# Kernel optimization log

Hardware: AMD Instinct MI355X
Metric: run time of the kernel (lower is better)

## Reference

```python
import jax, jax.numpy as jnp
from jax import lax
import numpy as np

EPS = 1e-6
D_KQ = 256  # per-head q/k dim; softmax scale = sqrt(256) = 16


def layernorm(x, g, b):
    m = jnp.mean(x, axis=-1, keepdims=True)
    v = jnp.var(x, axis=-1, keepdims=True)  # biased, matches torch LayerNorm
    return (x - m) / jnp.sqrt(v + EPS) * g + b


def lrelu(t):
    return jnp.where(t > 0, t, 0.1 * t)


def setup_inputs() -> dict:
    key = jax.random.key(0)
    ks = jax.random.split(key, 10)
    B, C, H, W = 256, 17, 84, 84
    d_model, heads = 512, 4
    hid = D_KQ * heads  # 1024
    out_dim = 256
    s = 0.05
    return {
        "x": jax.random.normal(ks[0], (B, C, H, W), jnp.float32),
        "conv1_w": jax.random.normal(ks[1], (64, C, 8, 8), jnp.float32) * s,
        "conv1_b": jnp.zeros((64,), jnp.float32),
        "conv2_w": jax.random.normal(ks[2], (510, 64, 4, 4), jnp.float32) * s,
        "conv2_b": jnp.zeros((510,), jnp.float32),
        "wq": jax.random.normal(ks[3], (hid, d_model), jnp.float32) * s,
        "wk": jax.random.normal(ks[4], (hid, d_model), jnp.float32) * s,
        "wv": jax.random.normal(ks[5], (hid, d_model), jnp.float32) * s,
        "ln_e_g": jnp.ones((hid,), jnp.float32),
        "ln_e_b": jnp.zeros((hid,), jnp.float32),
        "wo": jax.random.normal(ks[6], (d_model, hid), jnp.float32) * s,
        "ln_g": jnp.ones((d_model,), jnp.float32),
        "ln_b": jnp.zeros((d_model,), jnp.float32),
        "map_w": jax.random.normal(ks[7], (out_dim, d_model), jnp.float32) * s,
        "map_b": jnp.zeros((out_dim,), jnp.float32),
    }


def reference(x, conv1_w, conv1_b, conv2_w, conv2_b, wq, wk, wv,
              ln_e_g, ln_e_b, wo, ln_g, ln_b, map_w, map_b):
    dn = ("NCHW", "OIHW", "NCHW")
    # feature extractor
    y = lax.conv_general_dilated(x, conv1_w, (4, 4), "VALID", dimension_numbers=dn)
    y = lrelu(y + conv1_b[None, :, None, None])
    y = lax.conv_general_dilated(y, conv2_w, (2, 2), "VALID", dimension_numbers=dn)
    y = lrelu(y + conv2_b[None, :, None, None])  # [B,510,H2,W2]
    B, Cc, H2, W2 = y.shape
    N = H2 * W2
    e = jnp.transpose(y.reshape(B, Cc, N), (0, 2, 1))  # [B,N,510]
    # coordinate augmentation: [(i//W)/H, (i%W)/W]
    idx = jnp.arange(N)
    coord = jnp.stack([(idx // W2) / H2, (idx % W2) / W2], axis=-1).astype(e.dtype)
    e = jnp.concatenate([e, jnp.broadcast_to(coord, (B, N, 2))], axis=-1)  # [B,N,512]
    heads = 4
    # projections + per-projection LayerNorm over full hid dim (pre-head-split)
    q = layernorm(e @ wq.T, ln_e_g, ln_e_b).reshape(B, N, heads, D_KQ)
    k = layernorm(e @ wk.T, ln_e_g, ln_e_b).reshape(B, N, heads, D_KQ)
    v = layernorm(e @ wv.T, ln_e_g, ln_e_b).reshape(B, N, heads, D_KQ)
    scores = jnp.einsum("bnhd,bmhd->bhnm", q, k) / jnp.sqrt(jnp.float32(D_KQ))
    w = jax.nn.softmax(scores, axis=-1)
    nv = jnp.einsum("bhnm,bmhd->bnhd", w, v).reshape(B, N, heads * D_KQ)
    out = layernorm(nv @ wo.T + e, ln_g, ln_b)  # residual + LN
    out = jax.nn.relu(out)
    out = jnp.max(out, axis=1)  # maxout over entities -> [B,512]
    return lrelu(out @ map_w.T + map_b)  # mapping -> [B,256]
```

## Files before the change

### kernel.cpp

```cpp
#include <hip/hip_runtime.h>
#include <hip/hip_bf16.h>
#include <math.h>

typedef __hip_bfloat16 bf16;
using f32x4 = __attribute__((ext_vector_type(4))) float;
using s16x8 = __attribute__((ext_vector_type(8))) short;

#define DEV_INLINE __device__ __forceinline__

static constexpr int BB   = 256;
static constexpr int CIN  = 17;
static constexpr int WIN  = 84;
static constexpr int C1   = 64;
static constexpr int W1   = 20;
static constexpr int P1   = W1 * W1;
static constexpr int C2   = 510;
static constexpr int W2   = 9;
static constexpr int NE   = 81;
static constexpr int DM   = 512;
static constexpr int HID  = 1024;
static constexpr int NH   = 4;
static constexpr int DK   = 256;
static constexpr int MR   = BB * NE;
static constexpr int ODIM = 256;
static constexpr int PLANE = WIN * WIN;
static constexpr int QS   = 3 * HID;

DEV_INLINE float lrelu_f(float v) { return v > 0.f ? v : 0.1f * v; }
DEV_INLINE float bf2f(ushort u) { return __uint_as_float((unsigned)u << 16); }
DEV_INLINE short f2bs(float f) { bf16 t = __float2bfloat16(f); return *reinterpret_cast<short*>(&t); }

DEV_INLINE void gll16(const void* g, const void* l) {
    __builtin_amdgcn_global_load_lds(
        (const __attribute__((address_space(1))) unsigned int*)g,
        (__attribute__((address_space(3))) unsigned int*)l, 16, 0, 0);
}
DEV_INLINE f32x4 mfma16(s16x8 a, s16x8 b, f32x4 c) {
    return __builtin_amdgcn_mfma_f32_16x16x32_bf16(a, b, c, 0, 0, 0);
}

__global__ void k_prep(const float* __restrict__ w1, const float* __restrict__ w2,
        const float* __restrict__ b2, const float* __restrict__ wq,
        const float* __restrict__ wk, const float* __restrict__ wv,
        const float* __restrict__ wo, bf16* __restrict__ w1b,
        bf16* __restrict__ w2b, float* __restrict__ b2p,
        bf16* __restrict__ wqkv, bf16* __restrict__ wob) {
    int i = blockIdx.x * 256 + threadIdx.x;
    if (i < 17408) {
        const size_t o = (size_t)i * 4;
        const float4 v = *(const float4*)(w1 + o);
        short r[4] = { f2bs(v.x), f2bs(v.y), f2bs(v.z), f2bs(v.w) };
        *(ushort4*)(w1b + o) = *(ushort4*)r;
        return;
    }
    i -= 17408;
    if (i < 524288) {
        const int n = i >> 10, rem = i & 1023;
        const int khkw = rem >> 6, ic = rem & 63;
        w2b[i] = (n < C2) ? __float2bfloat16(w2[n * 1024 + ic * 16 + khkw])
                          : __float2bfloat16(0.f);
        return;
    }
    i -= 524288;
    if (i < 512) { b2p[i] = (i < C2) ? b2[i] : 0.f; return; }
    i -= 512;
    if (i < 393216) {
        const size_t o = (size_t)i * 4;
        const int n = (int)(o >> 9), c = (int)(o & 511);
        const float* src = (n < 1024) ? wq : (n < 2048) ? wk : wv;
        const float4 v = *(const float4*)(src + (size_t)(n & 1023) * 512 + c);
        short r[4] = { f2bs(v.x), f2bs(v.y), f2bs(v.z), f2bs(v.w) };
        *(ushort4*)(wqkv + o) = *(ushort4*)r;
        return;
    }
    i -= 393216;
    if (i < 131072) {
        const size_t o = (size_t)i * 4;
        const float4 v = *(const float4*)(wo + o);
        short r[4] = { f2bs(v.x), f2bs(v.y), f2bs(v.z), f2bs(v.w) };
        *(ushort4*)(wob + o) = *(ushort4*)r;
    }
}

__global__ __launch_bounds__(512, 1) void k_conv1_mfma(const float* __restrict__ x,
        const bf16* __restrict__ w1b, const float* __restrict__ bias,
        bf16* __restrict__ y1t) {
    __shared__ __align__(16) char pl[2][28224];
    const int b = blockIdx.x;
    const int tid = threadIdx.x;
    const int w = tid >> 6, l = tid & 63;
    const int l15 = l & 15, l4 = l >> 4;
    const float* xb = x + (size_t)b * CIN * PLANE;

    int baseA[4], tval[4];
    #pragma unroll
    for (int j = 0; j < 4; ++j) {
        const int t = w + 8 * j; tval[j] = t;
        int p = t * 16 + l15; if (t >= 25) p = 0;
        const int oh = p / 20, ow = p % 20;
        baseA[j] = (oh * 4 + l4) * 336 + ow * 16;
    }
    float bias_r[4];
    #pragma unroll
    for (int nt = 0; nt < 4; ++nt) bias_r[nt] = bias[nt * 16 + l15];

    #pragma unroll
    for (int it = 0; it < 4; ++it) {
        const int g = it * 512 + tid;
        if (g < 1764) gll16(xb + (size_t)g * 4, pl[0] + (size_t)g * 16);
    }
    __syncthreads();

    f32x4 acc[4][4] = {};
    int cur = 0;
    for (int ic = 0; ic < CIN; ++ic) {
        if (ic + 1 < CIN) {
            const float* src = xb + (size_t)(ic + 1) * PLANE;
            #pragma unroll
            for (int it = 0; it < 4; ++it) {
                const int g = it * 512 + tid;
                if (g < 1764) gll16(src + (size_t)g * 4, pl[cur ^ 1] + (size_t)g * 16);
            }
        }
        s16x8 bq[4][2];
        #pragma unroll
        for (int nt = 0; nt < 4; ++nt)
            #pragma unroll
            for (int ks = 0; ks < 2; ++ks)
                bq[nt][ks] = *(const s16x8*)(w1b + (size_t)(nt * 16 + l15) * 1088
                                             + ic * 64 + (ks * 4 + l4) * 8);
        const char* P = pl[cur];
        #pragma unroll
        for (int j = 0; j < 4; ++j) {
            if (tval[j] < 25) {
                #pragma unroll
                for (int ks = 0; ks < 2; ++ks) {
                    const float* fp = (const float*)(P + baseA[j] + ks * 1344);
                    const f32x4 f0 = *(const f32x4*)fp;
                    const f32x4 f1 = *(const f32x4*)(fp + 4);
                    s16x8 af;
                    #pragma unroll
                    for (int jj = 0; jj < 4; ++jj) {
                        af[jj]     = f2bs(f0[jj]);
                        af[jj + 4] = f2bs(f1[jj]);
                    }
                    #pragma unroll
                    for (int nt = 0; nt < 4; ++nt)
                        acc[j][nt] = mfma16(af, bq[nt][ks], acc[j][nt]);
                }
            }
        }
        __syncthreads();
        cur ^= 1;
    }
    #pragma unroll
    for (int j = 0; j < 4; ++j) {
        if (tval[j] < 25) {
            #pragma unroll
            for (int nt = 0; nt < 4; ++nt) {
                #pragma unroll
                for (int q = 0; q < 4; ++q) {
                    const int pix = tval[j] * 16 + l4 * 4 + q;
                    const int oc  = nt * 16 + l15;
                    y1t[((size_t)b * P1 + pix) * 64 + oc] =
                        __float2bfloat16(lrelu_f(acc[j][nt][q] + bias_r[nt]));
                }
            }
        }
    }
}

__global__ __launch_bounds__(256) void k_gemm_conv2(const bf16* __restrict__ A,
        const bf16* __restrict__ B, const float* __restrict__ bias,
        bf16* __restrict__ Cb) {
    __shared__ __align__(16) char Asm[2][128 * 64];
    __shared__ __align__(16) char Bsm[2][128 * 64];
    const int tid = threadIdx.x;
    const int m0 = blockIdx.y * 128, n0 = blockIdx.x * 128;
    const int w = tid >> 6, l = tid & 63;
    const int wm = w >> 1, wn = w & 1;
    const int l15 = l & 15, l4 = l >> 4;
    const int r0 = tid >> 2, p0 = tid & 3;
    const int r1 = 64 + r0;
    const int sw0 = (p0 ^ ((r0 >> 1) & 3)) << 3;
    const int sw1 = (p0 ^ ((r1 >> 1) & 3)) << 3;
    int bimg[2], ohh[2], oww[2];
    #pragma unroll
    for (int it = 0; it < 2; ++it) {
        const int m = m0 + (it ? r1 : r0);
        bimg[it] = m / 81;
        const int n = m - bimg[it] * 81;
        ohh[it] = n / 9; oww[it] = n - ohh[it] * 9;
    }
    auto stage = [&](int buf, int k0) {
        const int khkw = k0 >> 6, icb = k0 & 63;
        const int kh = khkw >> 2, kwv = khkw & 3;
        const int pix0 = (ohh[0] * 2 + kh) * 20 + oww[0] * 2 + kwv;
        const int pix1 = (ohh[1] * 2 + kh) * 20 + oww[1] * 2 + kwv;
        gll16(A + ((size_t)bimg[0] * P1 + pix0) * 64 + icb + sw0, Asm[buf] + tid * 16);
        gll16(A + ((size_t)bimg[1] * P1 + pix1) * 64 + icb + sw1, Asm[buf] + (256 + tid) * 16);
        gll16(B + (size_t)(n0 + r0) * HID + k0 + sw0, Bsm[buf] + tid * 16);
        gll16(B + (size_t)(n0 + r1) * HID + k0 + sw1, Bsm[buf] + (256 + tid) * 16);
    };
    stage(0, 0);
    __syncthreads();
    f32x4 acc[4][4] = {};
    int cur = 0;
    for (int t = 0; t < 32; ++t) {
        if (t < 31) stage(cur ^ 1, (t + 1) * 32);
        s16x8 af[4], bfv[4];
        #pragma unroll
        for (int i = 0; i < 4; ++i) {
            const int ra = wm * 64 + i * 16 + l15;
            af[i]  = *(const s16x8*)(Asm[cur] + ra * 64 + ((l4 ^ ((ra >> 1) & 3)) << 4));
            const int rb = wn * 64 + i * 16 + l15;
            bfv[i] = *(const s16x8*)(Bsm[cur] + rb * 64 + ((l4 ^ ((rb >> 1) & 3)) << 4));
        }
        #pragma unroll
        for (int i = 0; i < 4; ++i)
            #pragma unroll
            for (int j = 0; j < 4; ++j)
                acc[i][j] = mfma16(af[i], bfv[j], acc[i][j]);
        __syncthreads();
        cur ^= 1;
    }
    #pragma unroll
    for (int i = 0; i < 4; ++i) {
        #pragma unroll
        for (int j = 0; j < 4; ++j) {
            const int col = n0 + wn * 64 + j * 16 + l15;
            #pragma unroll
            for (int q = 0; q < 4; ++q) {
                const int row = m0 + wm * 64 + i * 16 + l4 * 4 + q;
                float v = lrelu_f(acc[i][j][q] + bias[col]);
                if (col >= 510) {
                    const int n = row % 81;
                    v = (col == 510) ? (float)(n / 9) * (1.f / 9.f)
                                     : (float)(n % 9) * (1.f / 9.f);
                }
                Cb[(size_t)row * DM + col] = __float2bfloat16(v);
            }
        }
    }
}

#define QKV_PHASE(QD, STAGING, TAIL)                                           \
    {                                                                          \
        s16x8 areg[2][2];                                                      \
        _Pragma("unroll")                                                      \
        for (int ii = 0; ii < 2; ++ii) {                                       \
            const int fr = QD * 32 + ii * 16 + l15;                            \
            _Pragma("unroll")                                                  \
            for (int kk = 0; kk < 2; ++kk)                                     \
                areg[ii][kk] = *(const s16x8*)(Abase + fr * 128 +              \
                                   (((kk * 4 + l4) ^ (fr & 7)) << 4));         \
        }                                                                      \
        STAGING;                                                               \
        __builtin_amdgcn_s_barrier();                                          \
        asm volatile("s_waitcnt lgkmcnt(0)" ::: "memory");                     \
        __builtin_amdgcn_sched_barrier(0);                                     \
        __builtin_amdgcn_s_setprio(1);                                         \
        _Pragma("unroll")                                                      \
        for (int ii = 0; ii < 2; ++ii)                                         \
            _Pragma("unroll")                                                  \
            for (int j = 0; j < 4; ++j)                                        \
                _Pragma("unroll")                                              \
                for (int kk = 0; kk < 2; ++kk)                                 \
                    acc[QD * 2 + ii][j] =                                      \
                        mfma16(areg[ii][kk], breg[j][kk], acc[QD * 2 + ii][j]);\
        __builtin_amdgcn_s_setprio(0);                                         \
        TAIL;                                                                  \
        __builtin_amdgcn_s_barrier();                                          \
        __builtin_amdgcn_sched_barrier(0);                                     \
    }

__global__ __launch_bounds__(512, 2) void k_gemm_qkv8(const bf16* __restrict__ A,
        const bf16* __restrict__ B, bf16* __restrict__ Cb,
        float2* __restrict__ part) {
    __shared__ __align__(16) char lds[131072];
    const int tid = threadIdx.x;
    const int m0 = blockIdx.y * 256, n0 = blockIdx.x * 256;
    const int wid = tid >> 6, l = tid & 63;
    const int wm = wid >> 2, wn = wid & 3;
    const int l15 = l & 15, l4 = l >> 4;
    const int rA = tid >> 3, pA = tid & 7;

    auto stageA = [&](int buf, int kt, int qa) {
        char* dst = lds + buf * 32768 + (qa >> 1) * 16384 + (qa & 1) * 8192 + tid * 16;
        gll16(A + (size_t)(m0 + qa * 64 + rA) * 512 + kt * 64 + ((pA ^ (rA & 7)) << 3), dst);
    };
    auto stageB = [&](int buf, int kt, int hb) {
        char* base = lds + 65536 + buf * 32768 + hb * 16384;
        #pragma unroll
        for (int i2 = 0; i2 < 2; ++i2) {
            const int s = i2 * 512 + tid;
            const int c = s >> 3, pp = s & 7;
            gll16(B + (size_t)(n0 + hb * 128 + c) * 512 + kt * 64 + ((pp ^ (c & 7)) << 3),
                  base + s * 16);
        }
    };

    stageA(0, 0, 0); stageA(0, 0, 1); stageA(0, 0, 2); stageA(0, 0, 3);
    stageB(0, 0, 0); stageB(0, 0, 1);
    stageB(1, 1, 0); stageB(1, 1, 1);
    stageA(1, 1, 0); stageA(1, 1, 2);
    asm volatile("s_waitcnt vmcnt(6)" ::: "memory");
    __builtin_amdgcn_s_barrier();
    __builtin_amdgcn_sched_barrier(0);

    f32x4 acc[8][4] = {};
    for (int kt = 0; kt < 8; ++kt) {
        const int cur = kt & 1;
        const char* Abase = lds + cur * 32768 + wm * 16384;
        const char* Bbase = lds + 65536 + cur * 32768 + (wn >> 1) * 16384;
        s16x8 breg[4][2];
        #pragma unroll
        for (int j = 0; j < 4; ++j) {
            const int fc = (wn & 1) * 64 + j * 16 + l15;
            #pragma unroll
            for (int kk = 0; kk < 2; ++kk)
                breg[j][kk] = *(const s16x8*)(Bbase + fc * 128 +
                                  (((kk * 4 + l4) ^ (fc & 7)) << 4));
        }
        QKV_PHASE(0, { if (kt + 1 < 8) { stageA(cur ^ 1, kt + 1, 1); stageA(cur ^ 1, kt + 1, 3); } }, {})
        QKV_PHASE(1, { if (kt + 2 < 8) { stageB(cur, kt + 2, 0); } }, {})
        QKV_PHASE(2, { if (kt + 2 < 8) { stageB(cur, kt + 2, 1); stageA(cur, kt + 2, 0); stageA(cur, kt + 2, 2); } }, {})
        QKV_PHASE(3, { }, {
            if (kt < 6)       { asm volatile("s_waitcnt vmcnt(6)" ::: "memory"); }
            else if (kt == 6) { asm volatile("s_waitcnt vmcnt(0)" ::: "memory"); }
        })
    }

    #pragma unroll
    for (int fi = 0; fi < 8; ++fi) {
        #pragma unroll
        for (int q = 0; q < 4; ++q) {
            const int row = m0 + wm * 128 + fi * 16 + l4 * 4 + q;
            float s = 0.f, s2 = 0.f;
            #pragma unroll
            for (int j = 0; j < 4; ++j) {
                const float v = acc[fi][j][q];
                s += v; s2 += v * v;
            }
            #pragma unroll
            for (int o = 1; o < 16; o <<= 1) {
                s  += __shfl_xor(s, o, 64);
                s2 += __shfl_xor(s2, o, 64);
            }
            if (l15 == 0)
                part[(size_t)row * 48 + blockIdx.x * 4 + wn] = make_float2(s, s2);
            bf16* cr = Cb + (size_t)row * QS + n0 + wn * 64;
            #pragma unroll
            for (int j = 0; j < 4; ++j)
                cr[j * 16 + l15] = __float2bfloat16(acc[fi][j][q]);
        }
    }
}

template <int RESID>
__global__ __launch_bounds__(256) void k_gemm_stats(const bf16* __restrict__ A,
        const bf16* __restrict__ B, const bf16* __restrict__ resid,
        bf16* __restrict__ Cb, float2* __restrict__ part,
        int K, int ldc, int nPH) {
    __shared__ __align__(16) char Asm[2][16384];
    __shared__ __align__(16) char Bsm[2][16384];
    const int tid = threadIdx.x;
    const int m0 = blockIdx.y * 128, n0 = blockIdx.x * 128;
    const int w = tid >> 6, l = tid & 63;
    const int wm = w >> 1, wn = w & 1;
    const int l15 = l & 15, l4 = l >> 4;

    auto stage = [&](int buf, int k0) {
        #pragma unroll
        for (int it = 0; it < 4; ++it) {
            const int g = it * 256 + tid;
            const int r = g >> 3, p = g & 7;
            const int sw = (p ^ (r & 7)) << 3;
            gll16(A + (size_t)(m0 + r) * K + k0 + sw, Asm[buf] + g * 16);
            gll16(B + (size_t)(n0 + r) * K + k0 + sw, Bsm[buf] + g * 16);
        }
    };
    stage(0, 0);
    __syncthreads();
    f32x4 acc[4][4] = {};
    int cur = 0;
    const int nt = K >> 6;
    for (int t = 0; t < nt; ++t) {
        if (t + 1 < nt) stage(cur ^ 1, (t + 1) * 64);
        #pragma unroll
        for (int kk = 0; kk < 2; ++kk) {
            s16x8 af[4], bfv[4];
            const int pz = kk * 4 + l4;
            #pragma unroll
            for (int i = 0; i < 4; ++i) {
                const int ra = wm * 64 + i * 16 + l15;
                af[i]  = *(const s16x8*)(Asm[cur] + ra * 128 + ((pz ^ (ra & 7)) << 4));
                const int rb = wn * 64 + i * 16 + l15;
                bfv[i] = *(const s16x8*)(Bsm[cur] + rb * 128 + ((pz ^ (rb & 7)) << 4));
            }
            #pragma unroll
            for (int i = 0; i < 4; ++i)
                #pragma unroll
                for (int j = 0; j < 4; ++j)
                    acc[i][j] = mfma16(af[i], bfv[j], acc[i][j]);
        }
        __syncthreads();
        cur ^= 1;
    }
    #pragma unroll
    for (int i = 0; i < 4; ++i) {
        #pragma unroll
        for (int q = 0; q < 4; ++q) {
            const int row = m0 + wm * 64 + i * 16 + l4 * 4 + q;
            if (RESID) {
                const bf16* rr = resid + (size_t)row * ldc;
                #pragma unroll
                for (int j = 0; j < 4; ++j)
                    acc[i][j][q] += bf2f(*(const ushort*)(rr + n0 + wn * 64 + j * 16 + l15));
            }
            float s = 0.f, s2 = 0.f;
            #pragma unroll
            for (int j = 0; j < 4; ++j) {
                const float v = acc[i][j][q];
                s += v; s2 += v * v;
            }
            #pragma unroll
            for (int o = 1; o < 16; o <<= 1) {
                s  += __shfl_xor(s, o, 64);
                s2 += __shfl_xor(s2, o, 64);
            }
            if (l15 == 0)
                part[(size_t)row * nPH + (n0 >> 6) + wn] = make_float2(s, s2);
            bf16* cr = Cb + (size_t)row * ldc + n0 + wn * 64;
            #pragma unroll
            for (int j = 0; j < 4; ++j)
                cr[j * 16 + l15] = __float2bfloat16(acc[i][j][q]);
        }
    }
}

__global__ void k_red(const float2* __restrict__ part, float2* __restrict__ stats,
                      int total, int nPH, int groups, float invD) {
    const int gid = blockIdx.x * 256 + threadIdx.x;
    if (gid >= total) return;
    const int proj = gid / MR, row = gid - proj * MR;
    const float2* p = part + (size_t)row * (nPH * groups) + proj * nPH;
    float s = 0.f, s2 = 0.f;
    for (int h = 0; h < nPH; ++h) { s += p[h].x; s2 += p[h].y; }
    const float mean = s * invD;
    const float var  = s2 * invD - mean * mean;
    stats[gid] = make_float2(mean, rsqrtf(var + 1e-6f));
}

__global__ __launch_bounds__(256) void k_vt(const bf16* __restrict__ qkv3,
        const float2* __restrict__ vstats, const float* __restrict__ g,
        const float* __restrict__ bprm, bf16* __restrict__ vt) {
    __shared__ bf16 T[81 * 264];
    const int tid = threadIdx.x;
    const int bh = blockIdx.x;
    const int b = bh >> 2, h = bh & 3;
    const int brow = b * NE;
    const int hoff = h * DK;
    for (int gidx = tid; gidx < 81 * 32; gidx += 256) {
        const int m = gidx >> 5, c8 = gidx & 31;
        const int row = brow + m;
        const s16x8 vv = *(const s16x8*)(qkv3 + (size_t)row * QS + 2048 + hoff + c8 * 8);
        const float2 st = vstats[row];
        const int col0 = hoff + c8 * 8;
        const float4 g0 = *(const float4*)(g + col0), g1 = *(const float4*)(g + col0 + 4);
        const float4 b0 = *(const float4*)(bprm + col0), b1 = *(const float4*)(bprm + col0 + 4);
        const float ga[8] = { g0.x, g0.y, g0.z, g0.w, g1.x, g1.y, g1.z, g1.w };
        const float ba[8] = { b0.x, b0.y, b0.z, b0.w, b1.x, b1.y, b1.z, b1.w };
        short o[8];
        #pragma unroll
        for (int jj = 0; jj < 8; ++jj) {
            const float a = st.y * ga[jj];
            o[jj] = f2bs(bf2f((ushort)vv[jj]) * a + (ba[jj] - st.x * a));
        }
        *(s16x8*)(T + m * 264 + c8 * 8) = *(s16x8*)o;
    }
    __syncthreads();
    const int d = tid;
    bf16 row[96];
    #pragma unroll
    for (int m = 0; m < 81; ++m) row[m] = T[m * 264 + d];
    #pragma unroll
    for (int m = 81; m < 96; ++m) row[m] = __float2bfloat16(0.f);
    bf16* out = vt + ((size_t)bh * DK + d) * 96;
    #pragma unroll
    for (int g8 = 0; g8 < 12; ++g8)
        *(s16x8*)(out + g8 * 8) = *(const s16x8*)(&row[g8 * 8]);
}

__global__ __launch_bounds__(512) void k_attn3(const bf16* __restrict__ qkv3,
        const float2* __restrict__ stats, const float* __restrict__ g,
        const float* __restrict__ bprm, const bf16* __restrict__ vt,
        bf16* __restrict__ nv) {
    __shared__ __align__(16) char smem[49152 + 96 * 104 * 2];
    char* Ks = smem;
    bf16* Pb = (bf16*)(smem + 49152);
    const int tid = threadIdx.x;
    const int bh = blockIdx.x;
    const int b = bh >> 2, h = bh & 3;
    const int brow = b * NE;
    const int hoff = h * DK;
    const int w = tid >> 6, l = tid & 63;
    const int l15 = l & 15, l4 = l >> 4;

    for (int gidx = tid; gidx < 96 * 32; gidx += 512) {
        const int r = gidx >> 5, c8 = gidx & 31;
        int krow = brow + r; if (krow >= MR) krow = MR - 1;
        const s16x8 kv = *(const s16x8*)(qkv3 + (size_t)krow * QS + 1024 + hoff + c8 * 8);
        const float2 st = stats[MR + krow];
        const int col0 = hoff + c8 * 8;
        const float4 g0 = *(const float4*)(g + col0), g1 = *(const float4*)(g + col0 + 4);
        const float4 b0 = *(const float4*)(bprm + col0), b1 = *(const float4*)(bprm + col0 + 4);
        const float ga[8] = { g0.x, g0.y, g0.z, g0.w, g1.x, g1.y, g1.z, g1.w };
        const float ba[8] = { b0.x, b0.y, b0.z, b0.w, b1.x, b1.y, b1.z, b1.w };
        short o[8];
        #pragma unroll
        for (int jj = 0; jj < 8; ++jj) {
            const float a = st.y * ga[jj];
            o[jj] = f2bs(bf2f((ushort)kv[jj]) * a + (ba[jj] - st.x * a));
        }
        *(s16x8*)(Ks + r * 512 + ((c8 ^ (r & 7)) << 4)) = *(s16x8*)o;
    }
    __syncthreads();

    if (w < 6) {
        int qrow = brow + w * 16 + l15; if (qrow >= MR) qrow = MR - 1;
        const float2 stq = stats[qrow];
        s16x8 qa[8];
        #pragma unroll
        for (int kk = 0; kk < 8; ++kk) {
            const int col0 = hoff + kk * 32 + l4 * 8;
            const s16x8 qv = *(const s16x8*)(qkv3 + (size_t)qrow * QS + col0);
            const float4 g0 = *(const float4*)(g + col0), g1 = *(const float4*)(g + col0 + 4);
            const float4 b0 = *(const float4*)(bprm + col0), b1 = *(const float4*)(bprm + col0 + 4);
            const float ga[8] = { g0.x, g0.y, g0.z, g0.w, g1.x, g1.y, g1.z, g1.w };
            const float ba[8] = { b0.x, b0.y, b0.z, b0.w, b1.x, b1.y, b1.z, b1.w };
            short o[8];
            #pragma unroll
            for (int jj = 0; jj < 8; ++jj) {
                const float a = stq.y * ga[jj];
                o[jj] = f2bs(bf2f((ushort)qv[jj]) * a + (ba[jj] - stq.x * a));
            }
            qa[kk] = *(s16x8*)o;
        }
        f32x4 sacc[6];
        #pragma unroll
        for (int j = 0; j < 6; ++j) {
            f32x4 a = {};
            const int rb = j * 16 + l15;
            #pragma unroll
            for (int kk = 0; kk < 8; ++kk) {
                const s16x8 kf = *(const s16x8*)(Ks + rb * 512 + (((kk * 4 + l4) ^ (rb & 7)) << 4));
                a = mfma16(qa[kk], kf, a);
            }
            sacc[j] = a;
        }
        float px[6][4];
        #pragma unroll
        for (int q = 0; q < 4; ++q) {
            float m = -1e30f;
            #pragma unroll
            for (int j = 0; j < 6; ++j) {
                const int key = j * 16 + l15;
                const float v = (key < NE) ? sacc[j][q] : -1e30f;
                px[j][q] = v;
                m = fmaxf(m, v);
            }
            #pragma unroll
            for (int o = 1; o < 16; o <<= 1) m = fmaxf(m, __shfl_xor(m, o, 64));
            float s = 0.f;
            #pragma unroll
            for (int j = 0; j < 6; ++j) {
                const float e = __expf((px[j][q] - m) * 0.0625f);
                px[j][q] = e; s += e;
            }
            #pragma unroll
            for (int o = 1; o < 16; o <<= 1) s += __shfl_xor(s, o, 64);
            const float r = 1.f / s;
            #pragma unroll
            for (int j = 0; j < 6; ++j) px[j][q] *= r;
        }
        #pragma unroll
        for (int j = 0; j < 6; ++j)
            #pragma unroll
            for (int q = 0; q < 4; ++q)
                Pb[(w * 16 + l4 * 4 + q) * 104 + j * 16 + l15] =
                    __float2bfloat16(px[j][q]);
    }
    __syncthreads();

    const bf16* vtb = vt + (size_t)bh * DK * 96;
    s16x8 vf[2][3];
    #pragma unroll
    for (int dj = 0; dj < 2; ++dj) {
        const int d = (2 * w + dj) * 16 + l15;
        #pragma unroll
        for (int ks = 0; ks < 3; ++ks)
            vf[dj][ks] = *(const s16x8*)(vtb + (size_t)d * 96 + (ks * 4 + l4) * 8);
    }
    f32x4 oacc[6][2] = {};
    #pragma unroll
    for (int i = 0; i < 6; ++i) {
        s16x8 pa[3];
        #pragma unroll
        for (int ks = 0; ks < 3; ++ks)
            pa[ks] = *(const s16x8*)(Pb + (i * 16 + l15) * 104 + (ks * 4 + l4) * 8);
        #pragma unroll
        for (int dj = 0; dj < 2; ++dj)
            #pragma unroll
            for (int ks = 0; ks < 3; ++ks)
                oacc[i][dj] = mfma16(pa[ks], vf[dj][ks], oacc[i][dj]);
    }
    #pragma unroll
    for (int i = 0; i < 6; ++i) {
        #pragma unroll
        for (int q = 0; q < 4; ++q) {
            const int n = i * 16 + l4 * 4 + q;
            if (n < NE) {
                #pragma unroll
                for (int dj = 0; dj < 2; ++dj) {
                    const int d = (2 * w + dj) * 16 + l15;
                    nv[(size_t)(brow + n) * HID + hoff + d] =
                        __float2bfloat16(oacc[i][dj][q]);
                }
            }
        }
    }
}

__global__ void k_maxpool_ln(const bf16* __restrict__ X, const float2* __restrict__ st,
        const float* __restrict__ g, const float* __restrict__ bprm,
        float* __restrict__ P) {
    const int i = blockIdx.x * 256 + threadIdx.x;
    const int bb = i >> 9, c = i & 511;
    const float gc = g[c], bc = bprm[c];
    const bf16* xp = X + (size_t)bb * NE * DM + c;
    const float2* sp = st + (size_t)bb * NE;
    float mx = -1e30f;
    for (int n = 0; n < NE; ++n) {
        const float2 s = sp[n];
        const float a = s.y * gc;
        const float v = __bfloat162float(xp[(size_t)n * DM]) * a + (bc - s.x * a);
        mx = fmaxf(mx, fmaxf(v, 0.f));
    }
    P[i] = mx;
}

__global__ __launch_bounds__(256) void k_final(const float* __restrict__ P,
        const float* __restrict__ W, const float* __restrict__ bias,
        float* __restrict__ out) {
    const int bb = blockIdx.x;
    __shared__ float pr[DM];
    for (int i = threadIdx.x; i < DM; i += 256) pr[i] = P[(size_t)bb * DM + i];
    __syncthreads();
    const int o = threadIdx.x;
    const float4* w4 = (const float4*)(W + (size_t)o * DM);
    float acc = 0.f;
    for (int c4 = 0; c4 < DM / 4; ++c4) {
        const float4 wv = w4[c4];
        acc += wv.x * pr[c4 * 4] + wv.y * pr[c4 * 4 + 1]
             + wv.z * pr[c4 * 4 + 2] + wv.w * pr[c4 * 4 + 3];
    }
    out[(size_t)bb * ODIM + o] = lrelu_f(acc + bias[o]);
}

extern "C" void kernel_launch(void* const* d_in, const int* in_sizes, int n_in,
                              void* d_out, int out_size, void* d_ws, size_t ws_size,
                              hipStream_t stream) {
    const float* x   = (const float*)d_in[0];
    const float* w1  = (const float*)d_in[1];
    const float* b1  = (const float*)d_in[2];
    const float* w2  = (const float*)d_in[3];
    const float* b2  = (const float*)d_in[4];
    const float* wq  = (const float*)d_in[5];
    const float* wk  = (const float*)d_in[6];
    const float* wvv = (const float*)d_in[7];
    const float* lng = (const float*)d_in[8];
    const float* lnb = (const float*)d_in[9];
    const float* wo  = (const float*)d_in[10];
    const float* lg2 = (const float*)d_in[11];
    const float* lb2 = (const float*)d_in[12];
    const float* mw  = (const float*)d_in[13];
    const float* mb  = (const float*)d_in[14];

    char* ws = (char*)d_ws;
    size_t off = 0;
    auto alloc = [&](size_t bytes) {
        void* p = ws + off;
        off = (off + bytes + 255) & ~(size_t)255;
        return p;
    };
    bf16*   y1t   = (bf16*)  alloc((size_t)BB * P1 * 64 * 2);
    bf16*   ebf   = (bf16*)  alloc((size_t)MR * DM * 2);
    bf16*   qkv3  = (bf16*)  alloc((size_t)MR * QS * 2);
    bf16*   vt    = (bf16*)  alloc((size_t)BB * NH * DK * 96 * 2);
    bf16*   nv    = (bf16*)  alloc((size_t)MR * HID * 2);
    bf16*   ao    = (bf16*)  alloc((size_t)MR * DM * 2);
    float*  pool  = (float*) alloc((size_t)BB * DM * 4);
    float2* part1 = (float2*)alloc((size_t)MR * 48 * 8);
    float2* part2 = (float2*)alloc((size_t)MR * 8 * 8);
    float2* stQKV = (float2*)alloc((size_t)3 * MR * 8);
    float2* st2   = (float2*)alloc((size_t)MR * 8);
    bf16*   w1b   = (bf16*)  alloc((size_t)C1 * CIN * 64 * 2);
    bf16*   w2b   = (bf16*)  alloc((size_t)512 * HID * 2);
    float*  b2p   = (float*) alloc(512 * 4);
    bf16*   wqkv  = (bf16*)  alloc((size_t)3072 * DM * 2);
    bf16*   wob   = (bf16*)  alloc((size_t)DM * HID * 2);
    float*  outp  = (float*)d_out;

    k_prep<<<4166, 256, 0, stream>>>(w1, w2, b2, wq, wk, wvv, wo,
                                     w1b, w2b, b2p, wqkv, wob);

    k_conv1_mfma<<<BB, 512, 0, stream>>>(x, w1b, b1, y1t);

    k_gemm_conv2<<<dim3(4, MR / 128), 256, 0, stream>>>(y1t, w2b, b2p, ebf);

    k_gemm_qkv8<<<dim3(12, MR / 256), 512, 0, stream>>>(ebf, wqkv, qkv3, part1);
    k_red<<<(3 * MR + 255) / 256, 256, 0, stream>>>(part1, stQKV, 3 * MR, 16, 3,
                                                    1.f / 1024.f);

    k_vt<<<BB * NH, 256, 0, stream>>>(qkv3, stQKV + 2 * MR, lng, lnb, vt);

    k_attn3<<<BB * NH, 512, 0, stream>>>(qkv3, stQKV, lng, lnb, vt, nv);

    k_gemm_stats<1><<<dim3(4, MR / 128), 256, 0, stream>>>(nv, wob, ebf,
                                                           ao, part2, HID, DM, 8);
    k_red<<<(MR + 255) / 256, 256, 0, stream>>>(part2, st2, MR, 8, 1, 1.f / 512.f);

    k_maxpool_ln<<<(BB * DM) / 256, 256, 0, stream>>>(ao, st2, lg2, lb2, pool);
    k_final<<<BB, 256, 0, stream>>>(pool, mw, mb, outp);
}
```

Before: 362.0 us.

## Fuse V normalization/transpose into attention and fuse maxpool with final mapping

```diff
diff --git a/kernel.cpp b/kernel.cpp
--- a/kernel.cpp
+++ b/kernel.cpp
@@ -452,53 +452,13 @@
     stats[gid] = make_float2(mean, rsqrtf(var + 1e-6f));
 }
 
-__global__ __launch_bounds__(256) void k_vt(const bf16* __restrict__ qkv3,
-        const float2* __restrict__ vstats, const float* __restrict__ g,
-        const float* __restrict__ bprm, bf16* __restrict__ vt) {
-    __shared__ bf16 T[81 * 264];
-    const int tid = threadIdx.x;
-    const int bh = blockIdx.x;
-    const int b = bh >> 2, h = bh & 3;
-    const int brow = b * NE;
-    const int hoff = h * DK;
-    for (int gidx = tid; gidx < 81 * 32; gidx += 256) {
-        const int m = gidx >> 5, c8 = gidx & 31;
-        const int row = brow + m;
-        const s16x8 vv = *(const s16x8*)(qkv3 + (size_t)row * QS + 2048 + hoff + c8 * 8);
-        const float2 st = vstats[row];
-        const int col0 = hoff + c8 * 8;
-        const float4 g0 = *(const float4*)(g + col0), g1 = *(const float4*)(g + col0 + 4);
-        const float4 b0 = *(const float4*)(bprm + col0), b1 = *(const float4*)(bprm + col0 + 4);
-        const float ga[8] = { g0.x, g0.y, g0.z, g0.w, g1.x, g1.y, g1.z, g1.w };
-        const float ba[8] = { b0.x, b0.y, b0.z, b0.w, b1.x, b1.y, b1.z, b1.w };
-        short o[8];
-        #pragma unroll
-        for (int jj = 0; jj < 8; ++jj) {
-            const float a = st.y * ga[jj];
-            o[jj] = f2bs(bf2f((ushort)vv[jj]) * a + (ba[jj] - st.x * a));
-        }
-        *(s16x8*)(T + m * 264 + c8 * 8) = *(s16x8*)o;
-    }
-    __syncthreads();
-    const int d = tid;
-    bf16 row[96];
-    #pragma unroll
-    for (int m = 0; m < 81; ++m) row[m] = T[m * 264 + d];
-    #pragma unroll
-    for (int m = 81; m < 96; ++m) row[m] = __float2bfloat16(0.f);
-    bf16* out = vt + ((size_t)bh * DK + d) * 96;
-    #pragma unroll
-    for (int g8 = 0; g8 < 12; ++g8)
-        *(s16x8*)(out + g8 * 8) = *(const s16x8*)(&row[g8 * 8]);
-}
-
-__global__ __launch_bounds__(512) void k_attn3(const bf16* __restrict__ qkv3,
+__global__ __launch_bounds__(512) void k_attn4(const bf16* __restrict__ qkv3,
         const float2* __restrict__ stats, const float* __restrict__ g,
-        const float* __restrict__ bprm, const bf16* __restrict__ vt,
-        bf16* __restrict__ nv) {
-    __shared__ __align__(16) char smem[49152 + 96 * 104 * 2];
+        const float* __restrict__ bprm, bf16* __restrict__ nv) {
+    __shared__ __align__(16) char smem[49152 + 96 * 104 * 2 + 81 * 264 * 2];
     char* Ks = smem;
     bf16* Pb = (bf16*)(smem + 49152);
+    char* Vs = smem + 49152 + 96 * 104 * 2;
     const int tid = threadIdx.x;
     const int bh = blockIdx.x;
     const int b = bh >> 2, h = bh & 3;
@@ -525,6 +485,24 @@
         }
         *(s16x8*)(Ks + r * 512 + ((c8 ^ (r & 7)) << 4)) = *(s16x8*)o;
     }
+    for (int gidx = tid; gidx < NE * 32; gidx += 512) {
+        const int m = gidx >> 5, c8 = gidx & 31;
+        const int row = brow + m;
+        const s16x8 vv = *(const s16x8*)(qkv3 + (size_t)row * QS + 2048 + hoff + c8 * 8);
+        const float2 st = stats[2 * MR + row];
+        const int col0 = hoff + c8 * 8;
+        const float4 g0 = *(const float4*)(g + col0), g1 = *(const float4*)(g + col0 + 4);
+        const float4 b0 = *(const float4*)(bprm + col0), b1 = *(const float4*)(bprm + col0 + 4);
+        const float ga[8] = { g0.x, g0.y, g0.z, g0.w, g1.x, g1.y, g1.z, g1.w };
+        const float ba[8] = { b0.x, b0.y, b0.z, b0.w, b1.x, b1.y, b1.z, b1.w };
+        short o[8];
+        #pragma unroll
+        for (int jj = 0; jj < 8; ++jj) {
+            const float a = st.y * ga[jj];
+            o[jj] = f2bs(bf2f((ushort)vv[jj]) * a + (ba[jj] - st.x * a));
+        }
+        *(s16x8*)(Vs + (size_t)(m * 264 + c8 * 8) * 2) = *(s16x8*)o;
+    }
     __syncthreads();
 
     if (w < 6) {
@@ -593,14 +571,19 @@
     }
     __syncthreads();
 
-    const bf16* vtb = vt + (size_t)bh * DK * 96;
     s16x8 vf[2][3];
     #pragma unroll
     for (int dj = 0; dj < 2; ++dj) {
         const int d = (2 * w + dj) * 16 + l15;
         #pragma unroll
-        for (int ks = 0; ks < 3; ++ks)
-            vf[dj][ks] = *(const s16x8*)(vtb + (size_t)d * 96 + (ks * 4 + l4) * 8);
+        for (int ks = 0; ks < 3; ++ks) {
+            #pragma unroll
+            for (int jj = 0; jj < 8; ++jj) {
+                const int m = (ks * 4 + l4) * 8 + jj;
+                vf[dj][ks][jj] = (m < NE)
+                    ? *(const short*)(Vs + (size_t)(m * 264 + d) * 2) : (short)0;
+            }
+        }
     }
     f32x4 oacc[6][2] = {};
     #pragma unroll
@@ -632,11 +615,13 @@
     }
 }
 
-__global__ void k_maxpool_ln(const bf16* __restrict__ X, const float2* __restrict__ st,
-        const float* __restrict__ g, const float* __restrict__ bprm,
-        float* __restrict__ P) {
-    const int i = blockIdx.x * 256 + threadIdx.x;
-    const int bb = i >> 9, c = i & 511;
+__global__ __launch_bounds__(512) void k_pool_final(const bf16* __restrict__ X,
+        const float2* __restrict__ st, const float* __restrict__ g,
+        const float* __restrict__ bprm, const float* __restrict__ W,
+        const float* __restrict__ bias, float* __restrict__ out) {
+    __shared__ float pr[DM];
+    const int bb = blockIdx.x;
+    const int c = threadIdx.x;
     const float gc = g[c], bc = bprm[c];
     const bf16* xp = X + (size_t)bb * NE * DM + c;
     const float2* sp = st + (size_t)bb * NE;
@@ -644,28 +629,22 @@
     for (int n = 0; n < NE; ++n) {
         const float2 s = sp[n];
         const float a = s.y * gc;
-        const float v = __bfloat162float(xp[(size_t)n * DM]) * a + (bc - s.x * a);
+        const float v = bf2f(*(const ushort*)(xp + (size_t)n * DM)) * a + (bc - s.x * a);
         mx = fmaxf(mx, fmaxf(v, 0.f));
     }
-    P[i] = mx;
-}
-
-__global__ __launch_bounds__(256) void k_final(const float* __restrict__ P,
-        const float* __restrict__ W, const float* __restrict__ bias,
-        float* __restrict__ out) {
-    const int bb = blockIdx.x;
-    __shared__ float pr[DM];
-    for (int i = threadIdx.x; i < DM; i += 256) pr[i] = P[(size_t)bb * DM + i];
+    pr[c] = mx;
     __syncthreads();
-    const int o = threadIdx.x;
-    const float4* w4 = (const float4*)(W + (size_t)o * DM);
-    float acc = 0.f;
-    for (int c4 = 0; c4 < DM / 4; ++c4) {
-        const float4 wv = w4[c4];
-        acc += wv.x * pr[c4 * 4] + wv.y * pr[c4 * 4 + 1]
-             + wv.z * pr[c4 * 4 + 2] + wv.w * pr[c4 * 4 + 3];
-    }
-    out[(size_t)bb * ODIM + o] = lrelu_f(acc + bias[o]);
+    if (c < ODIM) {
+        const float4* w4 = (const float4*)(W + (size_t)c * DM);
+        float acc = 0.f;
+        #pragma unroll 4
+        for (int c4 = 0; c4 < DM / 4; ++c4) {
+            const float4 wv = w4[c4];
+            acc += wv.x * pr[c4 * 4] + wv.y * pr[c4 * 4 + 1]
+                 + wv.z * pr[c4 * 4 + 2] + wv.w * pr[c4 * 4 + 3];
+        }
+        out[(size_t)bb * ODIM + c] = lrelu_f(acc + bias[c]);
+    }
 }
 
 extern "C" void kernel_launch(void* const* d_in, const int* in_sizes, int n_in,
@@ -697,10 +676,8 @@
     bf16*   y1t   = (bf16*)  alloc((size_t)BB * P1 * 64 * 2);
     bf16*   ebf   = (bf16*)  alloc((size_t)MR * DM * 2);
     bf16*   qkv3  = (bf16*)  alloc((size_t)MR * QS * 2);
-    bf16*   vt    = (bf16*)  alloc((size_t)BB * NH * DK * 96 * 2);
     bf16*   nv    = (bf16*)  alloc((size_t)MR * HID * 2);
     bf16*   ao    = (bf16*)  alloc((size_t)MR * DM * 2);
-    float*  pool  = (float*) alloc((size_t)BB * DM * 4);
     float2* part1 = (float2*)alloc((size_t)MR * 48 * 8);
     float2* part2 = (float2*)alloc((size_t)MR * 8 * 8);
     float2* stQKV = (float2*)alloc((size_t)3 * MR * 8);
@@ -723,14 +700,11 @@
     k_red<<<(3 * MR + 255) / 256, 256, 0, stream>>>(part1, stQKV, 3 * MR, 16, 3,
                                                     1.f / 1024.f);
 
-    k_vt<<<BB * NH, 256, 0, stream>>>(qkv3, stQKV + 2 * MR, lng, lnb, vt);
-
-    k_attn3<<<BB * NH, 512, 0, stream>>>(qkv3, stQKV, lng, lnb, vt, nv);
+    k_attn4<<<BB * NH, 512, 0, stream>>>(qkv3, stQKV, lng, lnb, nv);
 
     k_gemm_stats<1><<<dim3(4, MR / 128), 256, 0, stream>>>(nv, wob, ebf,
                                                            ao, part2, HID, DM, 8);
     k_red<<<(MR + 255) / 256, 256, 0, stream>>>(part2, st2, MR, 8, 1, 1.f / 512.f);
 
-    k_maxpool_ln<<<(BB * DM) / 256, 256, 0, stream>>>(ao, st2, lg2, lb2, pool);
-    k_final<<<BB, 256, 0, stream>>>(pool, mw, mb, outp);
-}
+    k_pool_final<<<BB, 512, 0, stream>>>(ao, st2, lg2, lb2, mw, mb, outp);
+}
```

Result: faster. 348.6 us (-3.7%).
